# Optimization experiments

Hardware: AMD Instinct MI355X
Metric: run time of the kernel (lower is better)

The kernel has to match this reference:

```python
import jax, jax.numpy as jnp
import numpy as np

N, K, C, G, B = 65536, 16, 64, 8, 4
PE_IN = 28  # 3 + 1 + 2*4*2 + 1*4*2
EPS = 1e-5
FREQS = (1.0, 2.0, 4.0, 8.0)  # 2 ** linspace(0, 3, 4)


def _bn(x, p):
    # inference-mode BatchNorm1d over last dim; p: [4, d] = (gamma, beta, mean, var)
    return (x - p[2]) * (p[0] / jnp.sqrt(p[3] + EPS)) + p[1]


def setup_inputs() -> dict:
    key = jax.random.key(0)
    ks = iter(jax.random.split(key, 48))

    def nrm(shape, s=0.05):
        return jax.random.normal(next(ks), shape, jnp.float32) * s

    def bnp(d):
        k1, k2, k3, k4 = jax.random.split(next(ks), 4)
        return jnp.stack([
            jax.random.uniform(k1, (d,), jnp.float32, 0.5, 1.5),   # gamma
            jax.random.normal(k2, (d,), jnp.float32) * 0.1,        # beta
            jax.random.normal(k3, (d,), jnp.float32) * 0.1,        # running mean
            jax.random.uniform(k4, (d,), jnp.float32, 0.5, 1.5),   # running var
        ])

    return dict(
        feat=nrm((N, C), 1.0),
        coord=jax.random.normal(next(ks), (N, 3), jnp.float32),
        reference_index=jax.random.randint(next(ks), (N, K), 0, N),
        offset=jnp.array([N // 4, N // 2, 3 * N // 4, N], dtype=jnp.int32),
        Wq=nrm((C, C)), bq=nrm((C,)), bnq=bnp(C),
        Wk=nrm((C, C)), bk=nrm((C,)), bnk=bnp(C),
        Wv=nrm((C, C)), bv=nrm((C,)),
        pe_W1=nrm((PE_IN, C)), pe_b1=nrm((C,)), pe_bn=bnp(C),
        pe_W2=nrm((C, C)), pe_b2=nrm((C,)),
        we_W1=nrm((C, G)), we_b1=nrm((G,)), we_bn=bnp(G),
        we_W2=nrm((G, G)), we_b2=nrm((G,)),
        cg_W1=nrm((3 * C, C)), cg_b1=nrm((C,)), cg_bn=bnp(C),
        cg_W2=nrm((C, G), 0.001), cg_b2=jnp.full((G,), 3.0, jnp.float32),
    )


def reference(feat, coord, reference_index, offset, Wq, bq, bnq, Wk, bk, bnk,
              Wv, bv, pe_W1, pe_b1, pe_bn, pe_W2, pe_b2,
              we_W1, we_b1, we_bn, we_W2, we_b2,
              cg_W1, cg_b1, cg_bn, cg_W2, cg_b2):
    n = feat.shape[0]
    q = jax.nn.relu(_bn(feat @ Wq + bq, bnq))          # [N, C]
    k = jax.nn.relu(_bn(feat @ Wk + bk, bnk))          # [N, C]
    v = feat @ Wv + bv                                 # [N, C]

    idx = reference_index                              # [N, K]; -1 = pad
    idx_safe = jnp.maximum(idx, 0)
    key_feat = k[idx_safe]                             # [N, K, C] gather
    neighbor_xyz = coord[idx_safe]                     # [N, K, 3]
    value_g = v[idx_safe]                              # [N, K, C]

    delta = neighbor_xyz - coord[:, None, :]           # [N, K, 3]
    # Anisotropic Fourier relative position encoding
    x = delta.reshape(-1, 3)
    d_xy, d_z = x[:, :2], x[:, 2:3]
    dist = jnp.linalg.norm(x, axis=1, keepdims=True)
    feats = [x, dist]
    for f in FREQS:
        feats += [jnp.sin(d_xy * (f * np.pi)), jnp.cos(d_xy * (f * np.pi))]
    for f in FREQS:
        feats += [jnp.sin(d_z * (f * np.pi)), jnp.cos(d_z * (f * np.pi))]
    xe = jnp.concatenate(feats, axis=1)                # [N*K, 28]
    rpe = jax.nn.relu(_bn(xe @ pe_W1 + pe_b1, pe_bn)) @ pe_W2 + pe_b2
    rpe = rpe.reshape(n, idx.shape[1], -1)             # [N, K, C]

    relation = key_feat - q[:, None, :] + rpe          # [N, K, C]
    geom_w = jax.nn.relu(_bn(relation @ we_W1 + we_b1, we_bn)) @ we_W2 + we_b2  # [N, K, G]

    neighbor_ctx = q[idx_safe].max(axis=1)             # [N, C]
    seg = jnp.searchsorted(offset, jnp.arange(n), side='right')
    seg_max = jax.ops.segment_max(q, seg, num_segments=offset.shape[0])
    global_ctx = seg_max[seg]                          # [N, C] offset-wise global max pool

    gate_in = jnp.concatenate([q, neighbor_ctx, global_ctx], axis=-1)  # [N, 3C]
    gate = jax.nn.sigmoid(
        jax.nn.relu(_bn(gate_in @ cg_W1 + cg_b1, cg_bn)) @ cg_W2 + cg_b2)  # [N, G]

    attn = jax.nn.softmax(geom_w * gate[:, None, :], axis=1)  # softmax over K
    mask = jnp.sign(idx + 1).astype(attn.dtype)        # [N, K]
    attn = attn * mask[:, :, None]

    vg = value_g.reshape(n, idx.shape[1], G, -1)       # [N, K, G, C//G]
    out = jnp.einsum('nkgi,nkg->ngi', vg, attn)
    return out.reshape(n, -1)
```

## Files before the change

kernel.cpp:

```cpp
#include <hip/hip_runtime.h>
#include <hip/hip_bf16.h>

#define EPSF 1e-5f

typedef __attribute__((ext_vector_type(8))) short short8;
typedef __attribute__((ext_vector_type(4))) float f32x4;

__device__ __forceinline__ int seg_of(int i, int o0, int o1, int o2) {
    return (i >= o0) + (i >= o1) + (i >= o2);
}

__device__ __forceinline__ unsigned short f2bf(float f) {
    unsigned int u = __float_as_uint(f);
    unsigned int r = (u + 0x7fffu + ((u >> 16) & 1u)) >> 16;
    return (unsigned short)r;
}
__device__ __forceinline__ unsigned int pack2bf(float a, float b) {
    return (unsigned int)f2bf(a) | ((unsigned int)f2bf(b) << 16);
}
__device__ __forceinline__ float bflo(unsigned int u) { return __uint_as_float(u << 16); }
__device__ __forceinline__ float bfhi(unsigned int u) { return __uint_as_float(u & 0xffff0000u); }

__device__ __forceinline__ void stage_rows_bf16(const unsigned short* __restrict__ src,
                                                unsigned short* dst, int l) {
    int row = l >> 2, cq = (l & 3) * 16;
    const short8* s = (const short8*)(src + (size_t)row*64 + cq);
    short8* d0 = (short8*)(dst + row*72 + cq);
    d0[0] = s[0];
    d0[1] = s[1];
}

__device__ __forceinline__ void stage_rows_f32(const float* __restrict__ src,
                                               unsigned short* dst, int l) {
    int row = l >> 2, cq = (l & 3) * 16;
    const float4* s = (const float4*)(src + (size_t)row*64 + cq);
    unsigned int* d = (unsigned int*)(dst + row*72 + cq);
    #pragma unroll
    for (int i = 0; i < 4; ++i) {
        float4 f = s[i];
        d[i*2]   = pack2bf(f.x, f.y);
        d[i*2+1] = pack2bf(f.z, f.w);
    }
}

__global__ __launch_bounds__(256) void k_prep(
    const float* __restrict__ pe_W1, const float* __restrict__ pe_b1, const float* __restrict__ pe_bn,
    const float* __restrict__ pe_W2, const float* __restrict__ pe_b2,
    const float* __restrict__ we_W1, const float* __restrict__ we_b1, const float* __restrict__ we_bn,
    const float* __restrict__ cg_W1, const float* __restrict__ cg_b1, const float* __restrict__ cg_bn,
    const float* __restrict__ Wq, const float* __restrict__ bq, const float* __restrict__ bnq,
    const float* __restrict__ Wk, const float* __restrict__ bk, const float* __restrict__ bnk,
    const float* __restrict__ Wv,
    float* __restrict__ peb1f, float* __restrict__ cvecg, float* __restrict__ cgb1f,
    float* __restrict__ biasqF, float* __restrict__ biaskF, float* __restrict__ cgW1cF,
    unsigned short* __restrict__ WqF, unsigned short* __restrict__ WkF, unsigned short* __restrict__ WvF,
    unsigned short* __restrict__ weW1F, unsigned short* __restrict__ cgW1aF,
    unsigned short* __restrict__ cgW1bF,
    unsigned short* __restrict__ W1frag, unsigned short* __restrict__ Wcfrag)
{
    int t = threadIdx.x;
    __shared__ float sc1[64], csc[64], sqv[64], skv[64], wsc[8], wsh[8];
    __shared__ float sWe[64][8], sWb[8], sWc[64][8];
    if (t < 64) {
        float g = pe_bn[t], b = pe_bn[64+t], m = pe_bn[128+t], v = pe_bn[192+t];
        float s = g / sqrtf(v + EPSF);
        sc1[t] = s; peb1f[t] = pe_b1[t]*s + (b - m*s);
        g = cg_bn[t]; b = cg_bn[64+t]; m = cg_bn[128+t]; v = cg_bn[192+t];
        s = g / sqrtf(v + EPSF);
        csc[t] = s; cgb1f[t] = cg_b1[t]*s + (b - m*s);
        g = bnq[t]; b = bnq[64+t]; m = bnq[128+t]; v = bnq[192+t];
        s = g / sqrtf(v + EPSF);
        sqv[t] = s; biasqF[t] = bq[t]*s + (b - m*s);
        g = bnk[t]; b = bnk[64+t]; m = bnk[128+t]; v = bnk[192+t];
        s = g / sqrtf(v + EPSF);
        skv[t] = s; biaskF[t] = bk[t]*s + (b - m*s);
    }
    if (t < 8) {
        float g = we_bn[t], b = we_bn[8+t], m = we_bn[16+t], v = we_bn[24+t];
        float s = g / sqrtf(v + EPSF);
        wsc[t] = s; wsh[t] = b - m*s;
    }
    __syncthreads();
    for (int u = t; u < 512; u += 256) { int g = u & 7; sWe[u >> 3][g] = we_W1[u] * wsc[g]; }
    if (t < 8) sWb[t] = we_b1[t] * wsc[t] + wsh[t];
    __syncthreads();
    for (int u = t; u < 512; u += 256) {
        int h = u >> 3, g = u & 7;
        float a = 0.f;
        for (int c = 0; c < 64; ++c) a += pe_W2[h*64 + c] * sWe[c][g];
        sWc[h][g] = a;
    }
    if (t < 8) {
        float a = sWb[t];
        for (int c = 0; c < 64; ++c) a += pe_b2[c] * sWe[c][t];
        cvecg[t] = a;
    }
    __syncthreads();
    for (int u = t; u < 4096; u += 256) {
        int tile = u >> 9, l = (u >> 3) & 63, j = u & 7;
        int col = (tile >> 1)*16 + (l & 15);
        int kk  = (tile & 1)*32 + (l >> 4)*8 + j;
        WqF[u]    = f2bf(Wq[kk*64 + col] * sqv[col]);
        WkF[u]    = f2bf(Wk[kk*64 + col] * skv[col]);
        WvF[u]    = f2bf(Wv[kk*64 + col]);
        cgW1aF[u] = f2bf(cg_W1[kk*64 + col] * csc[col]);
        cgW1bF[u] = f2bf(cg_W1[(64 + kk)*64 + col] * csc[col]);
    }
    for (int u = t; u < 1024; u += 256) {
        int tile = u >> 9, l = (u >> 3) & 63, j = u & 7;
        int col = l & 15;
        int kk  = tile*32 + (l >> 4)*8 + j;
        weW1F[u] = (col < 8) ? f2bf(sWe[kk][col]) : 0;
    }
    for (int u = t; u < 4096; u += 256) {
        int k = u >> 6, c = u & 63;
        cgW1cF[u] = cg_W1[(128 + k)*64 + c] * csc[c];
    }
    {
        int ct = t >> 6, l = t & 63;
        int col = 16*ct + (l & 15), kg = l >> 4;
        #pragma unroll
        for (int j = 0; j < 8; ++j) {
            int k = kg*8 + j;
            float v = (k < 28) ? pe_W1[k*64 + col] * sc1[col] : 0.f;
            W1frag[ct*512 + l*8 + j] = f2bf(v);
        }
    }
    if (t < 128) {
        int kg = t >> 6, l = t & 63, g = l & 15;
        #pragma unroll
        for (int j = 0; j < 8; ++j) {
            int k = kg*32 + (l >> 4)*8 + j;
            float v = (g < 8) ? sWc[k][g] : 0.f;
            Wcfrag[kg*512 + l*8 + j] = f2bf(v);
        }
    }
}

__global__ __launch_bounds__(256) void k_prep2(
    const float* __restrict__ cg_W2, const float* __restrict__ we_W2,
    unsigned short* __restrict__ cgW2F, unsigned short* __restrict__ W2frag)
{
    int t = threadIdx.x;
    for (int u = t; u < 1024; u += 256) {
        int tile = u >> 9, l = (u >> 3) & 63, j = u & 7;
        int col = l & 15;
        int kk  = tile*32 + (l >> 4)*8 + j;
        cgW2F[u] = (col < 8) ? f2bf(cg_W2[kk*8 + col]) : 0;
    }
    if (t < 64) {
        int l = t, g = l & 15;
        #pragma unroll
        for (int j = 0; j < 8; ++j) {
            float v = (l < 16 && g < 8) ? we_W2[j*8 + g] : 0.f;
            W2frag[l*8 + j] = f2bf(v);
        }
    }
}

__global__ __launch_bounds__(256) void k_qkv(
    const float* __restrict__ feat, const int* __restrict__ offs,
    const unsigned short* __restrict__ WqF, const unsigned short* __restrict__ WkF,
    const unsigned short* __restrict__ WvF, const unsigned short* __restrict__ weW1F,
    const float* __restrict__ biasqF, const float* __restrict__ biaskF,
    const float* __restrict__ bv,
    unsigned short* __restrict__ v_bf, unsigned short* __restrict__ q_bf,
    float* __restrict__ kw, float* __restrict__ qw, float* __restrict__ seg_max)
{
    __shared__ unsigned short sF[4][16*72];
    __shared__ unsigned short sQ[4][16*72];
    __shared__ unsigned short sK[4][16*72];
    __shared__ float sSeg[64];

    int t = threadIdx.x, w = t >> 6, l = t & 63;
    int lc = l & 15, lg = l >> 4;
    int rblk = blockIdx.x * 64;
    int r0 = rblk + w * 16;
    int o0 = offs[0], o1 = offs[1], o2 = offs[2];
    bool fast = seg_of(rblk, o0,o1,o2) == seg_of(rblk + 63, o0,o1,o2);

    if (t < 64) sSeg[t] = 0.f;
    __syncthreads();

    stage_rows_f32(feat + (size_t)r0*64, sF[w], l);
    short8 a0 = *(const short8*)(sF[w] + lc*72 + lg*8);
    short8 a1 = *(const short8*)(sF[w] + lc*72 + 32 + lg*8);

    float bqc[4], bkc[4], bvc[4];
    #pragma unroll
    for (int ct = 0; ct < 4; ++ct) {
        bqc[ct] = biasqF[ct*16 + lc];
        bkc[ct] = biaskF[ct*16 + lc];
        bvc[ct] = bv[ct*16 + lc];
    }

    #pragma unroll
    for (int ct = 0; ct < 4; ++ct) {
        f32x4 z = {0.f,0.f,0.f,0.f};
        short8 b0 = *(const short8*)(WqF + (ct*2+0)*512 + l*8);
        short8 b1 = *(const short8*)(WqF + (ct*2+1)*512 + l*8);
        f32x4 c = __builtin_amdgcn_mfma_f32_16x16x32_bf16(a0, b0, z, 0,0,0);
        c = __builtin_amdgcn_mfma_f32_16x16x32_bf16(a1, b1, c, 0,0,0);
        float cmax = 0.f;
        #pragma unroll
        for (int reg = 0; reg < 4; ++reg) {
            float qv = fmaxf(c[reg] + bqc[ct], 0.f);
            sQ[w][(lg*4 + reg)*72 + ct*16 + lc] = f2bf(qv);
            if (fast) cmax = fmaxf(cmax, qv);
            else atomicMax((unsigned int*)&seg_max[seg_of(r0 + lg*4 + reg,o0,o1,o2)*64 + ct*16 + lc],
                           __float_as_uint(qv));
        }
        if (fast) {
            cmax = fmaxf(cmax, __shfl_xor(cmax, 16));
            cmax = fmaxf(cmax, __shfl_xor(cmax, 32));
            if (lg == 0)
                atomicMax((unsigned int*)&sSeg[ct*16 + lc], __float_as_uint(cmax));
        }
    }
    #pragma unroll
    for (int ct = 0; ct < 4; ++ct) {
        f32x4 z = {0.f,0.f,0.f,0.f};
        short8 b0 = *(const short8*)(WkF + (ct*2+0)*512 + l*8);
        short8 b1 = *(const short8*)(WkF + (ct*2+1)*512 + l*8);
        f32x4 c = __builtin_amdgcn_mfma_f32_16x16x32_bf16(a0, b0, z, 0,0,0);
        c = __builtin_amdgcn_mfma_f32_16x16x32_bf16(a1, b1, c, 0,0,0);
        #pragma unroll
        for (int reg = 0; reg < 4; ++reg)
            sK[w][(lg*4 + reg)*72 + ct*16 + lc] = f2bf(fmaxf(c[reg] + bkc[ct], 0.f));
    }
    #pragma unroll
    for (int ct = 0; ct < 4; ++ct) {
        f32x4 z = {0.f,0.f,0.f,0.f};
        short8 b0 = *(const short8*)(WvF + (ct*2+0)*512 + l*8);
        short8 b1 = *(const short8*)(WvF + (ct*2+1)*512 + l*8);
        f32x4 c = __builtin_amdgcn_mfma_f32_16x16x32_bf16(a0, b0, z, 0,0,0);
        c = __builtin_amdgcn_mfma_f32_16x16x32_bf16(a1, b1, c, 0,0,0);
        #pragma unroll
        for (int reg = 0; reg < 4; ++reg)
            sF[w][(lg*4 + reg)*72 + ct*16 + lc] = f2bf(c[reg] + bvc[ct]);
    }
    {
        short8 wb0 = *(const short8*)(weW1F + l*8);
        short8 wb1 = *(const short8*)(weW1F + 512 + l*8);
        short8 aq0 = *(const short8*)(sQ[w] + lc*72 + lg*8);
        short8 aq1 = *(const short8*)(sQ[w] + lc*72 + 32 + lg*8);
        short8 ak0 = *(const short8*)(sK[w] + lc*72 + lg*8);
        short8 ak1 = *(const short8*)(sK[w] + lc*72 + 32 + lg*8);
        f32x4 z = {0.f,0.f,0.f,0.f};
        f32x4 cq = __builtin_amdgcn_mfma_f32_16x16x32_bf16(aq0, wb0, z, 0,0,0);
        cq = __builtin_amdgcn_mfma_f32_16x16x32_bf16(aq1, wb1, cq, 0,0,0);
        f32x4 ck = __builtin_amdgcn_mfma_f32_16x16x32_bf16(ak0, wb0, z, 0,0,0);
        ck = __builtin_amdgcn_mfma_f32_16x16x32_bf16(ak1, wb1, ck, 0,0,0);
        if (lc < 8) {
            #pragma unroll
            for (int reg = 0; reg < 4; ++reg) {
                qw[(size_t)(r0 + lg*4 + reg)*8 + lc] = cq[reg];
                kw[(size_t)(r0 + lg*4 + reg)*8 + lc] = ck[reg];
            }
        }
    }
    #pragma unroll
    for (int rep = 0; rep < 2; ++rep) {
        int row = (l >> 3) + rep*8;
        int ch = (l & 7) * 8;
        short8 vq = *(const short8*)(sQ[w] + row*72 + ch);
        *(short8*)(q_bf + (size_t)(r0 + row)*64 + ch) = vq;
        short8 vv = *(const short8*)(sF[w] + row*72 + ch);
        *(short8*)(v_bf + (size_t)(r0 + row)*64 + ch) = vv;
    }
    __syncthreads();
    if (fast && t < 64)
        atomicMax((unsigned int*)&seg_max[seg_of(rblk,o0,o1,o2)*64 + t],
                  __float_as_uint(sSeg[t]));
}

__global__ __launch_bounds__(256) void k_seg(
    const float* __restrict__ seg_max, const float* __restrict__ cgW1cF,
    const float* __restrict__ cgb1f, float* __restrict__ gseg2)
{
    int t = threadIdx.x;
    int c = t & 63, s = t >> 6;
    float a = cgb1f[c];
    for (int j = 0; j < 64; ++j) a += seg_max[s*64 + j] * cgW1cF[j*64 + c];
    gseg2[s*64 + c] = a;
}

__global__ __launch_bounds__(256) void k_gate(
    const unsigned short* __restrict__ q_bf, const int* __restrict__ ridx,
    const unsigned short* __restrict__ cgW1aF, const unsigned short* __restrict__ cgW1bF,
    const unsigned short* __restrict__ cgW2F,
    const float* __restrict__ gseg2, const float* __restrict__ cg_b2,
    const int* __restrict__ offs,
    float* __restrict__ gate)
{
    __shared__ unsigned short sX[4][16*72];
    __shared__ unsigned short sN[4][16*72];
    __shared__ int sIdx[4][256];
    int t = threadIdx.x, w = t >> 6, l = t & 63;
    int lc = l & 15, lg = l >> 4;
    int r0 = blockIdx.x * 64 + w * 16;
    int o0 = offs[0], o1 = offs[1], o2 = offs[2];

    stage_rows_bf16(q_bf + (size_t)r0*64, sX[w], l);
    #pragma unroll
    for (int i = 0; i < 4; ++i)
        sIdx[w][l*4 + i] = ridx[(size_t)r0*16 + l*4 + i];

    short8 a0 = *(const short8*)(sX[w] + lc*72 + lg*8);
    short8 a1 = *(const short8*)(sX[w] + lc*72 + 32 + lg*8);

    {
        int row = l >> 2, cq = (l & 3) * 16;
        float m[16];
        #pragma unroll
        for (int i = 0; i < 16; ++i) m[i] = 0.f;
        for (int k = 0; k < 16; ++k) {
            int id = max(sIdx[w][row*16 + k], 0);
            const uint4* p = (const uint4*)(q_bf + (size_t)id*64 + cq);
            uint4 u0 = p[0], u1 = p[1];
            m[0]  = fmaxf(m[0],  bflo(u0.x)); m[1]  = fmaxf(m[1],  bfhi(u0.x));
            m[2]  = fmaxf(m[2],  bflo(u0.y)); m[3]  = fmaxf(m[3],  bfhi(u0.y));
            m[4]  = fmaxf(m[4],  bflo(u0.z)); m[5]  = fmaxf(m[5],  bfhi(u0.z));
            m[6]  = fmaxf(m[6],  bflo(u0.w)); m[7]  = fmaxf(m[7],  bfhi(u0.w));
            m[8]  = fmaxf(m[8],  bflo(u1.x)); m[9]  = fmaxf(m[9],  bfhi(u1.x));
            m[10] = fmaxf(m[10], bflo(u1.y)); m[11] = fmaxf(m[11], bfhi(u1.y));
            m[12] = fmaxf(m[12], bflo(u1.z)); m[13] = fmaxf(m[13], bfhi(u1.z));
            m[14] = fmaxf(m[14], bflo(u1.w)); m[15] = fmaxf(m[15], bfhi(u1.w));
        }
        unsigned int* d = (unsigned int*)(sN[w] + row*72 + cq);
        #pragma unroll
        for (int i = 0; i < 8; ++i) d[i] = pack2bf(m[2*i], m[2*i+1]);
    }

    f32x4 c4[4];
    #pragma unroll
    for (int ct = 0; ct < 4; ++ct) {
        #pragma unroll
        for (int reg = 0; reg < 4; ++reg)
            c4[ct][reg] = gseg2[seg_of(r0 + lg*4 + reg,o0,o1,o2)*64 + ct*16 + lc];
        short8 b0 = *(const short8*)(cgW1aF + (ct*2+0)*512 + l*8);
        short8 b1 = *(const short8*)(cgW1aF + (ct*2+1)*512 + l*8);
        c4[ct] = __builtin_amdgcn_mfma_f32_16x16x32_bf16(a0, b0, c4[ct], 0,0,0);
        c4[ct] = __builtin_amdgcn_mfma_f32_16x16x32_bf16(a1, b1, c4[ct], 0,0,0);
    }
    short8 n0v = *(const short8*)(sN[w] + lc*72 + lg*8);
    short8 n1v = *(const short8*)(sN[w] + lc*72 + 32 + lg*8);
    #pragma unroll
    for (int ct = 0; ct < 4; ++ct) {
        short8 b0 = *(const short8*)(cgW1bF + (ct*2+0)*512 + l*8);
        short8 b1 = *(const short8*)(cgW1bF + (ct*2+1)*512 + l*8);
        c4[ct] = __builtin_amdgcn_mfma_f32_16x16x32_bf16(n0v, b0, c4[ct], 0,0,0);
        c4[ct] = __builtin_amdgcn_mfma_f32_16x16x32_bf16(n1v, b1, c4[ct], 0,0,0);
        #pragma unroll
        for (int reg = 0; reg < 4; ++reg)
            sX[w][(lg*4 + reg)*72 + ct*16 + lc] = f2bf(fmaxf(c4[ct][reg], 0.f));
    }
    {
        short8 ah0 = *(const short8*)(sX[w] + lc*72 + lg*8);
        short8 ah1 = *(const short8*)(sX[w] + lc*72 + 32 + lg*8);
        short8 w0 = *(const short8*)(cgW2F + l*8);
        short8 w1 = *(const short8*)(cgW2F + 512 + l*8);
        float bg = cg_b2[lc & 7];
        f32x4 cg;
        #pragma unroll
        for (int reg = 0; reg < 4; ++reg) cg[reg] = bg;
        cg = __builtin_amdgcn_mfma_f32_16x16x32_bf16(ah0, w0, cg, 0,0,0);
        cg = __builtin_amdgcn_mfma_f32_16x16x32_bf16(ah1, w1, cg, 0,0,0);
        if (lc < 8) {
            #pragma unroll
            for (int reg = 0; reg < 4; ++reg)
                gate[(size_t)(r0 + lg*4 + reg)*8 + lc] = 1.f / (1.f + __expf(-cg[reg]));
        }
    }
}

__global__ __launch_bounds__(64, 4) void k_main(
    const float* __restrict__ coord, const int* __restrict__ ridx,
    const unsigned short* __restrict__ v_bf,
    const float* __restrict__ kw, const float* __restrict__ qw,
    const float* __restrict__ gate,
    const float* __restrict__ peb1f, const float* __restrict__ cvecg,
    const float* __restrict__ we_b2,
    const unsigned short* __restrict__ W1frag, const unsigned short* __restrict__ Wcfrag,
    const unsigned short* __restrict__ W2frag,
    float* __restrict__ out)
{
    __shared__ __align__(16) unsigned short sA1[64*40];
    __shared__ __align__(16) unsigned short sA2[16*72];
    __shared__ __align__(16) unsigned short sAh2[16*8];
    __shared__ float sAttn[4][16][9];
    __shared__ int sIds[64];

    int l = threadIdx.x;
    int pair = blockIdx.x * 64 + l;
    int nself = pair >> 4;

    int id = ridx[pair];
    sIds[l] = id;
    int ids = max(id, 0);

    {
        float cx = coord[nself*3], cy = coord[nself*3+1], cz = coord[nself*3+2];
        float dx = coord[ids*3]   - cx;
        float dy = coord[ids*3+1] - cy;
        float dz = coord[ids*3+2] - cz;
        float dist = sqrtf(dx*dx + dy*dy + dz*dz);
        unsigned int* row = (unsigned int*)sA1 + l*20;
        row[0] = pack2bf(dx, dy);
        row[1] = pack2bf(dz, dist);
        float sx, cx2, sy, cy2, sz, cz2;
        __sincosf(dx * 3.14159265358979f, &sx, &cx2);
        __sincosf(dy * 3.14159265358979f, &sy, &cy2);
        __sincosf(dz * 3.14159265358979f, &sz, &cz2);
        row[2]  = pack2bf(sx, sy);
        row[3]  = pack2bf(cx2, cy2);
        row[10] = pack2bf(sz, cz2);
        #pragma unroll
        for (int fi = 1; fi < 4; ++fi) {
            float nsx = 2.f*sx*cx2, ncx = fmaf(-2.f*sx, sx, 1.f);
            float nsy = 2.f*sy*cy2, ncy = fmaf(-2.f*sy, sy, 1.f);
            float nsz = 2.f*sz*cz2, ncz = fmaf(-2.f*sz, sz, 1.f);
            row[2 + 2*fi] = pack2bf(nsx, nsy);
            row[3 + 2*fi] = pack2bf(ncx, ncy);
            row[10 + fi]  = pack2bf(nsz, ncz);
            sx = nsx; cx2 = ncx; sy = nsy; cy2 = ncy; sz = nsz; cz2 = ncz;
        }
        row[14] = 0u; row[15] = 0u;
    }

    int lc = l & 15, lg = l >> 4;

    short8 bW1[4], bWc[2], bW2;
    #pragma unroll
    for (int ct = 0; ct < 4; ++ct) bW1[ct] = *(const short8*)(W1frag + ct*512 + l*8);
    bWc[0] = *(const short8*)(Wcfrag + l*8);
    bWc[1] = *(const short8*)(Wcfrag + 512 + l*8);
    bW2 = *(const short8*)(W2frag + l*8);

    float bias1[4];
    #pragma unroll
    for (int ct = 0; ct < 4; ++ct) bias1[ct] = peb1f[16*ct + lc];
    int g7 = lc & 7;
    float cvec_g = cvecg[g7];
    float bias3 = we_b2[g7];

    #pragma unroll
    for (int rt = 0; rt < 4; ++rt) {
        int n = blockIdx.x * 4 + rt;
        short8 a1 = *(const short8*)(sA1 + (rt*16 + lc)*40 + lg*8);
        f32x4 c1[4];
        #pragma unroll
        for (int ct = 0; ct < 4; ++ct) {
            f32x4 z = {0.f, 0.f, 0.f, 0.f};
            c1[ct] = __builtin_amdgcn_mfma_f32_16x16x32_bf16(a1, bW1[ct], z, 0, 0, 0);
        }
        #pragma unroll
        for (int ct = 0; ct < 4; ++ct) {
            #pragma unroll
            for (int reg = 0; reg < 4; ++reg) {
                float h1 = fmaxf(c1[ct][reg] + bias1[ct], 0.f);
                sA2[(lg*4 + reg)*72 + 16*ct + lc] = f2bf(h1);
            }
        }
        int ids_r[4];
        #pragma unroll
        for (int reg = 0; reg < 4; ++reg) ids_r[reg] = sIds[rt*16 + lg*4 + reg];
        float qwv = qw[(size_t)n*8 + g7];
        f32x4 c2;
        #pragma unroll
        for (int reg = 0; reg < 4; ++reg)
            c2[reg] = kw[(size_t)max(ids_r[reg],0)*8 + g7] - qwv + cvec_g;
        short8 a20 = *(const short8*)(sA2 + lc*72 + lg*8);
        short8 a21 = *(const short8*)(sA2 + lc*72 + 32 + lg*8);
        c2 = __builtin_amdgcn_mfma_f32_16x16x32_bf16(a20, bWc[0], c2, 0, 0, 0);
        c2 = __builtin_amdgcn_mfma_f32_16x16x32_bf16(a21, bWc[1], c2, 0, 0, 0);
        if (lc < 8) {
            #pragma unroll
            for (int reg = 0; reg < 4; ++reg)
                sAh2[(lg*4 + reg)*8 + lc] = f2bf(fmaxf(c2[reg], 0.f));
        }
        short8 a3 = {0,0,0,0,0,0,0,0};
        if (l < 16) a3 = *(const short8*)(sAh2 + lc*8);
        f32x4 c3;
        #pragma unroll
        for (int reg = 0; reg < 4; ++reg) c3[reg] = bias3;
        c3 = __builtin_amdgcn_mfma_f32_16x16x32_bf16(a3, bW2, c3, 0, 0, 0);
        float gv = gate[(size_t)n*8 + g7];
        float lgt[4];
        #pragma unroll
        for (int reg = 0; reg < 4; ++reg) lgt[reg] = c3[reg] * gv;
        float m = fmaxf(fmaxf(lgt[0], lgt[1]), fmaxf(lgt[2], lgt[3]));
        m = fmaxf(m, __shfl_xor(m, 16));
        m = fmaxf(m, __shfl_xor(m, 32));
        float e[4], s = 0.f;
        #pragma unroll
        for (int reg = 0; reg < 4; ++reg) { e[reg] = __expf(lgt[reg] - m); s += e[reg]; }
        s += __shfl_xor(s, 16);
        s += __shfl_xor(s, 32);
        float inv = 1.f / s;
        if (lc < 8) {
            #pragma unroll
            for (int reg = 0; reg < 4; ++reg) {
                int idv = ids_r[reg];
                float mf = (idv >= 0) ? 1.f : ((idv == -1) ? 0.f : -1.f);
                sAttn[rt][lg*4 + reg][lc] = e[reg] * inv * mf;
            }
        }
    }

    {
        int p = lg, kk = lc;
        int n2 = blockIdx.x * 4 + p;
        float4 o = make_float4(0.f, 0.f, 0.f, 0.f);
        int gh = kk >> 1;
        #pragma unroll
        for (int k2 = 0; k2 < 16; ++k2) {
            int id2 = max(sIds[p*16 + k2], 0);
            float a = sAttn[p][k2][gh];
            uint2 u = *(const uint2*)(v_bf + (size_t)id2*64 + kk*4);
            o.x += a * bflo(u.x); o.y += a * bfhi(u.x);
            o.z += a * bflo(u.y); o.w += a * bfhi(u.y);
        }
        *(float4*)(out + (size_t)n2*64 + kk*4) = o;
    }
}

extern "C" void kernel_launch(void* const* d_in, const int* in_sizes, int n_in,
                              void* d_out, int out_size, void* d_ws, size_t ws_size,
                              hipStream_t stream)
{
    const float* feat  = (const float*)d_in[0];
    const float* coord = (const float*)d_in[1];
    const int*   ridx  = (const int*)d_in[2];
    const int*   offs  = (const int*)d_in[3];
    const float* Wq = (const float*)d_in[4];  const float* bq = (const float*)d_in[5];  const float* bnq = (const float*)d_in[6];
    const float* Wk = (const float*)d_in[7];  const float* bk = (const float*)d_in[8];  const float* bnk = (const float*)d_in[9];
    const float* Wv = (const float*)d_in[10]; const float* bv = (const float*)d_in[11];
    const float* pe_W1 = (const float*)d_in[12]; const float* pe_b1 = (const float*)d_in[13]; const float* pe_bn = (const float*)d_in[14];
    const float* pe_W2 = (const float*)d_in[15]; const float* pe_b2 = (const float*)d_in[16];
    const float* we_W1 = (const float*)d_in[17]; const float* we_b1 = (const float*)d_in[18]; const float* we_bn = (const float*)d_in[19];
    const float* we_W2 = (const float*)d_in[20]; const float* we_b2 = (const float*)d_in[21];
    const float* cg_W1 = (const float*)d_in[22]; const float* cg_b1 = (const float*)d_in[23]; const float* cg_bn = (const float*)d_in[24];
    const float* cg_W2 = (const float*)d_in[25]; const float* cg_b2 = (const float*)d_in[26];
    float* out = (float*)d_out;
    int N = in_sizes[0] / 64;

    unsigned short* v_bf = (unsigned short*)d_ws;
    unsigned short* q_bf = v_bf + (size_t)N*64;
    float* kwp   = (float*)(q_bf + (size_t)N*64);
    float* qwp   = kwp + (size_t)N*8;
    float* gatep = qwp + (size_t)N*8;
    float* segm  = gatep + (size_t)N*8;
    float* gseg2 = segm + 256;
    float* peb1f = gseg2 + 256;
    float* cvecg = peb1f + 64;
    float* cgb1f = cvecg + 8;
    float* biasqF= cgb1f + 64;
    float* biaskF= biasqF + 64;
    float* pad0  = biaskF + 64;
    float* cgW1cF= pad0 + 56;
    unsigned short* WqF     = (unsigned short*)(cgW1cF + 4096);
    unsigned short* WkF     = WqF + 4096;
    unsigned short* WvF     = WkF + 4096;
    unsigned short* weW1F   = WvF + 4096;
    unsigned short* cgW1aF  = weW1F + 1024;
    unsigned short* cgW1bF  = cgW1aF + 4096;
    unsigned short* cgW2F   = cgW1bF + 4096;
    unsigned short* W1frag  = cgW2F + 1024;
    unsigned short* Wcfrag  = W1frag + 2048;
    unsigned short* W2frag  = Wcfrag + 1024;

    hipMemsetAsync(segm, 0, 256 * sizeof(float), stream);
    k_prep<<<1, 256, 0, stream>>>(pe_W1, pe_b1, pe_bn, pe_W2, pe_b2,
                                  we_W1, we_b1, we_bn,
                                  cg_W1, cg_b1, cg_bn,
                                  Wq, bq, bnq, Wk, bk, bnk, Wv,
                                  peb1f, cvecg, cgb1f, biasqF, biaskF, cgW1cF,
                                  WqF, WkF, WvF, weW1F, cgW1aF, cgW1bF,
                                  W1frag, Wcfrag);
    k_prep2<<<1, 256, 0, stream>>>(cg_W2, we_W2, cgW2F, W2frag);
    k_qkv<<<N/64, 256, 0, stream>>>(feat, offs, WqF, WkF, WvF, weW1F,
                                    biasqF, biaskF, bv,
                                    v_bf, q_bf, kwp, qwp, segm);
    k_seg<<<1, 256, 0, stream>>>(segm, cgW1cF, cgb1f, gseg2);
    k_gate<<<N/64, 256, 0, stream>>>(q_bf, ridx, cgW1aF, cgW1bF, cgW2F,
                                     gseg2, cg_b2, offs, gatep);
    k_main<<<N/4, 64, 0, stream>>>(coord, ridx, v_bf, kwp, qwp, gatep,
                                   peb1f, cvecg, we_b2,
                                   W1frag, Wcfrag, W2frag, out);
}
```

Baseline: 107.0 us.

## Fuse gate computation into main attention kernel with 256-thread blocks

Merges the separate k_gate kernel into k_main, so the context gate for each block of 16 points is computed in shared memory and read directly, with no round trip of the gate array through global memory. k_main grows from 64-thread blocks handling 4 points to 256-thread blocks handling 16 points, and the four waves split the gate's first-layer column tiles between them. This saves one launch plus the gate write and read, at the cost of extra __syncthreads barriers, more shared memory and changed occupancy (launch bounds 256,3).

```diff
diff --git a/kernel.cpp b/kernel.cpp
--- a/kernel.cpp
+++ b/kernel.cpp
@@ -285,127 +285,45 @@
     gseg2[s*64 + c] = a;
 }
 
-__global__ __launch_bounds__(256) void k_gate(
-    const unsigned short* __restrict__ q_bf, const int* __restrict__ ridx,
+__global__ __launch_bounds__(256, 3) void k_main(
+    const float* __restrict__ coord, const int* __restrict__ ridx,
+    const unsigned short* __restrict__ v_bf, const unsigned short* __restrict__ q_bf,
+    const float* __restrict__ kw, const float* __restrict__ qw,
+    const float* __restrict__ peb1f, const float* __restrict__ cvecg,
+    const float* __restrict__ we_b2, const float* __restrict__ cg_b2,
+    const float* __restrict__ gseg2, const int* __restrict__ offs,
+    const unsigned short* __restrict__ W1frag, const unsigned short* __restrict__ Wcfrag,
+    const unsigned short* __restrict__ W2frag,
     const unsigned short* __restrict__ cgW1aF, const unsigned short* __restrict__ cgW1bF,
     const unsigned short* __restrict__ cgW2F,
-    const float* __restrict__ gseg2, const float* __restrict__ cg_b2,
-    const int* __restrict__ offs,
-    float* __restrict__ gate)
+    float* __restrict__ out)
 {
-    __shared__ unsigned short sX[4][16*72];
-    __shared__ unsigned short sN[4][16*72];
-    __shared__ int sIdx[4][256];
+    __shared__ __align__(16) unsigned short sA1[256*40];
+    __shared__ __align__(16) unsigned short sA2[4][16*72];
+    __shared__ __align__(16) unsigned short sAh2[4][128];
+    __shared__ float sAttn[4][4][16][9];
+    __shared__ int sIds[256];
+    __shared__ __align__(16) unsigned short sQg[16*72];
+    __shared__ __align__(16) unsigned short sN[16*72];
+    __shared__ __align__(16) unsigned short sHg[16*72];
+    __shared__ float sGate[16][9];
+
     int t = threadIdx.x, w = t >> 6, l = t & 63;
     int lc = l & 15, lg = l >> 4;
-    int r0 = blockIdx.x * 64 + w * 16;
+    int n0 = blockIdx.x * 16;
     int o0 = offs[0], o1 = offs[1], o2 = offs[2];
 
-    stage_rows_bf16(q_bf + (size_t)r0*64, sX[w], l);
-    #pragma unroll
-    for (int i = 0; i < 4; ++i)
-        sIdx[w][l*4 + i] = ridx[(size_t)r0*16 + l*4 + i];
-
-    short8 a0 = *(const short8*)(sX[w] + lc*72 + lg*8);
-    short8 a1 = *(const short8*)(sX[w] + lc*72 + 32 + lg*8);
-
-    {
-        int row = l >> 2, cq = (l & 3) * 16;
-        float m[16];
-        #pragma unroll
-        for (int i = 0; i < 16; ++i) m[i] = 0.f;
-        for (int k = 0; k < 16; ++k) {
-            int id = max(sIdx[w][row*16 + k], 0);
-            const uint4* p = (const uint4*)(q_bf + (size_t)id*64 + cq);
-            uint4 u0 = p[0], u1 = p[1];
-            m[0]  = fmaxf(m[0],  bflo(u0.x)); m[1]  = fmaxf(m[1],  bfhi(u0.x));
-            m[2]  = fmaxf(m[2],  bflo(u0.y)); m[3]  = fmaxf(m[3],  bfhi(u0.y));
-            m[4]  = fmaxf(m[4],  bflo(u0.z)); m[5]  = fmaxf(m[5],  bfhi(u0.z));
-            m[6]  = fmaxf(m[6],  bflo(u0.w)); m[7]  = fmaxf(m[7],  bfhi(u0.w));
-            m[8]  = fmaxf(m[8],  bflo(u1.x)); m[9]  = fmaxf(m[9],  bfhi(u1.x));
-            m[10] = fmaxf(m[10], bflo(u1.y)); m[11] = fmaxf(m[11], bfhi(u1.y));
-            m[12] = fmaxf(m[12], bflo(u1.z)); m[13] = fmaxf(m[13], bfhi(u1.z));
-            m[14] = fmaxf(m[14], bflo(u1.w)); m[15] = fmaxf(m[15], bfhi(u1.w));
-        }
-        unsigned int* d = (unsigned int*)(sN[w] + row*72 + cq);
-        #pragma unroll
-        for (int i = 0; i < 8; ++i) d[i] = pack2bf(m[2*i], m[2*i+1]);
-    }
-
-    f32x4 c4[4];
-    #pragma unroll
-    for (int ct = 0; ct < 4; ++ct) {
-        #pragma unroll
-        for (int reg = 0; reg < 4; ++reg)
-            c4[ct][reg] = gseg2[seg_of(r0 + lg*4 + reg,o0,o1,o2)*64 + ct*16 + lc];
-        short8 b0 = *(const short8*)(cgW1aF + (ct*2+0)*512 + l*8);
-        short8 b1 = *(const short8*)(cgW1aF + (ct*2+1)*512 + l*8);
-        c4[ct] = __builtin_amdgcn_mfma_f32_16x16x32_bf16(a0, b0, c4[ct], 0,0,0);
-        c4[ct] = __builtin_amdgcn_mfma_f32_16x16x32_bf16(a1, b1, c4[ct], 0,0,0);
-    }
-    short8 n0v = *(const short8*)(sN[w] + lc*72 + lg*8);
-    short8 n1v = *(const short8*)(sN[w] + lc*72 + 32 + lg*8);
-    #pragma unroll
-    for (int ct = 0; ct < 4; ++ct) {
-        short8 b0 = *(const short8*)(cgW1bF + (ct*2+0)*512 + l*8);
-        short8 b1 = *(const short8*)(cgW1bF + (ct*2+1)*512 + l*8);
-        c4[ct] = __builtin_amdgcn_mfma_f32_16x16x32_bf16(n0v, b0, c4[ct], 0,0,0);
-        c4[ct] = __builtin_amdgcn_mfma_f32_16x16x32_bf16(n1v, b1, c4[ct], 0,0,0);
-        #pragma unroll
-        for (int reg = 0; reg < 4; ++reg)
-            sX[w][(lg*4 + reg)*72 + ct*16 + lc] = f2bf(fmaxf(c4[ct][reg], 0.f));
-    }
-    {
-        short8 ah0 = *(const short8*)(sX[w] + lc*72 + lg*8);
-        short8 ah1 = *(const short8*)(sX[w] + lc*72 + 32 + lg*8);
-        short8 w0 = *(const short8*)(cgW2F + l*8);
-        short8 w1 = *(const short8*)(cgW2F + 512 + l*8);
-        float bg = cg_b2[lc & 7];
-        f32x4 cg;
-        #pragma unroll
-        for (int reg = 0; reg < 4; ++reg) cg[reg] = bg;
-        cg = __builtin_amdgcn_mfma_f32_16x16x32_bf16(ah0, w0, cg, 0,0,0);
-        cg = __builtin_amdgcn_mfma_f32_16x16x32_bf16(ah1, w1, cg, 0,0,0);
-        if (lc < 8) {
-            #pragma unroll
-            for (int reg = 0; reg < 4; ++reg)
-                gate[(size_t)(r0 + lg*4 + reg)*8 + lc] = 1.f / (1.f + __expf(-cg[reg]));
-        }
-    }
-}
-
-__global__ __launch_bounds__(64, 4) void k_main(
-    const float* __restrict__ coord, const int* __restrict__ ridx,
-    const unsigned short* __restrict__ v_bf,
-    const float* __restrict__ kw, const float* __restrict__ qw,
-    const float* __restrict__ gate,
-    const float* __restrict__ peb1f, const float* __restrict__ cvecg,
-    const float* __restrict__ we_b2,
-    const unsigned short* __restrict__ W1frag, const unsigned short* __restrict__ Wcfrag,
-    const unsigned short* __restrict__ W2frag,
-    float* __restrict__ out)
-{
-    __shared__ __align__(16) unsigned short sA1[64*40];
-    __shared__ __align__(16) unsigned short sA2[16*72];
-    __shared__ __align__(16) unsigned short sAh2[16*8];
-    __shared__ float sAttn[4][16][9];
-    __shared__ int sIds[64];
-
-    int l = threadIdx.x;
-    int pair = blockIdx.x * 64 + l;
-    int nself = pair >> 4;
-
-    int id = ridx[pair];
-    sIds[l] = id;
+    int id = ridx[(size_t)n0*16 + t];
+    sIds[t] = id;
     int ids = max(id, 0);
-
+    int nself = n0 + (t >> 4);
     {
         float cx = coord[nself*3], cy = coord[nself*3+1], cz = coord[nself*3+2];
         float dx = coord[ids*3]   - cx;
         float dy = coord[ids*3+1] - cy;
         float dz = coord[ids*3+2] - cz;
         float dist = sqrtf(dx*dx + dy*dy + dz*dz);
-        unsigned int* row = (unsigned int*)sA1 + l*20;
+        unsigned int* row = (unsigned int*)sA1 + t*20;
         row[0] = pack2bf(dx, dy);
         row[1] = pack2bf(dz, dist);
         float sx, cx2, sy, cy2, sz, cz2;
@@ -427,9 +345,76 @@
         }
         row[14] = 0u; row[15] = 0u;
     }
-
-    int lc = l & 15, lg = l >> 4;
-
+    if (t < 64) stage_rows_bf16(q_bf + (size_t)n0*64, sQg, t);
+    __syncthreads();
+
+    {
+        int p = t >> 4, s = t & 15;
+        const int* ip = &sIds[p*16];
+        float m0 = 0.f, m1 = 0.f, m2 = 0.f, m3 = 0.f;
+        #pragma unroll
+        for (int kb = 0; kb < 16; kb += 4) {
+            uint2 u[4];
+            #pragma unroll
+            for (int j = 0; j < 4; ++j) {
+                int idn = max(ip[kb + j], 0);
+                u[j] = *(const uint2*)(q_bf + (size_t)idn*64 + s*4);
+            }
+            #pragma unroll
+            for (int j = 0; j < 4; ++j) {
+                m0 = fmaxf(m0, bflo(u[j].x)); m1 = fmaxf(m1, bfhi(u[j].x));
+                m2 = fmaxf(m2, bflo(u[j].y)); m3 = fmaxf(m3, bfhi(u[j].y));
+            }
+        }
+        unsigned int* d = (unsigned int*)(sN + p*72 + s*4);
+        d[0] = pack2bf(m0, m1);
+        d[1] = pack2bf(m2, m3);
+    }
+    __syncthreads();
+
+    {
+        short8 a0 = *(const short8*)(sQg + lc*72 + lg*8);
+        short8 a1 = *(const short8*)(sQg + lc*72 + 32 + lg*8);
+        short8 nv0 = *(const short8*)(sN + lc*72 + lg*8);
+        short8 nv1 = *(const short8*)(sN + lc*72 + 32 + lg*8);
+        f32x4 c4;
+        #pragma unroll
+        for (int reg = 0; reg < 4; ++reg)
+            c4[reg] = gseg2[seg_of(n0 + lg*4 + reg, o0, o1, o2)*64 + w*16 + lc];
+        short8 b0 = *(const short8*)(cgW1aF + (w*2+0)*512 + l*8);
+        short8 b1 = *(const short8*)(cgW1aF + (w*2+1)*512 + l*8);
+        c4 = __builtin_amdgcn_mfma_f32_16x16x32_bf16(a0, b0, c4, 0,0,0);
+        c4 = __builtin_amdgcn_mfma_f32_16x16x32_bf16(a1, b1, c4, 0,0,0);
+        short8 b2 = *(const short8*)(cgW1bF + (w*2+0)*512 + l*8);
+        short8 b3 = *(const short8*)(cgW1bF + (w*2+1)*512 + l*8);
+        c4 = __builtin_amdgcn_mfma_f32_16x16x32_bf16(nv0, b2, c4, 0,0,0);
+        c4 = __builtin_amdgcn_mfma_f32_16x16x32_bf16(nv1, b3, c4, 0,0,0);
+        #pragma unroll
+        for (int reg = 0; reg < 4; ++reg)
+            sHg[(lg*4 + reg)*72 + w*16 + lc] = f2bf(fmaxf(c4[reg], 0.f));
+    }
+    __syncthreads();
+
+    if (w == 0) {
+        short8 ah0 = *(const short8*)(sHg + lc*72 + lg*8);
+        short8 ah1 = *(const short8*)(sHg + lc*72 + 32 + lg*8);
+        short8 w0f = *(const short8*)(cgW2F + l*8);
+        short8 w1f = *(const short8*)(cgW2F + 512 + l*8);
+        float bg = cg_b2[lc & 7];
+        f32x4 cg;
+        #pragma unroll
+        for (int reg = 0; reg < 4; ++reg) cg[reg] = bg;
+        cg = __builtin_amdgcn_mfma_f32_16x16x32_bf16(ah0, w0f, cg, 0,0,0);
+        cg = __builtin_amdgcn_mfma_f32_16x16x32_bf16(ah1, w1f, cg, 0,0,0);
+        if (lc < 8) {
+            #pragma unroll
+            for (int reg = 0; reg < 4; ++reg)
+                sGate[lg*4 + reg][lc] = 1.f / (1.f + __expf(-cg[reg]));
+        }
+    }
+    __syncthreads();
+
+    int g7 = lc & 7;
     short8 bW1[4], bWc[2], bW2;
     #pragma unroll
     for (int ct = 0; ct < 4; ++ct) bW1[ct] = *(const short8*)(W1frag + ct*512 + l*8);
@@ -440,14 +425,13 @@
     float bias1[4];
     #pragma unroll
     for (int ct = 0; ct < 4; ++ct) bias1[ct] = peb1f[16*ct + lc];
-    int g7 = lc & 7;
     float cvec_g = cvecg[g7];
     float bias3 = we_b2[g7];
 
     #pragma unroll
     for (int rt = 0; rt < 4; ++rt) {
-        int n = blockIdx.x * 4 + rt;
-        short8 a1 = *(const short8*)(sA1 + (rt*16 + lc)*40 + lg*8);
+        int n = n0 + w*4 + rt;
+        short8 a1 = *(const short8*)(sA1 + (w*64 + rt*16 + lc)*40 + lg*8);
         f32x4 c1[4];
         #pragma unroll
         for (int ct = 0; ct < 4; ++ct) {
@@ -459,33 +443,33 @@
             #pragma unroll
             for (int reg = 0; reg < 4; ++reg) {
                 float h1 = fmaxf(c1[ct][reg] + bias1[ct], 0.f);
-                sA2[(lg*4 + reg)*72 + 16*ct + lc] = f2bf(h1);
+                sA2[w][(lg*4 + reg)*72 + 16*ct + lc] = f2bf(h1);
             }
         }
         int ids_r[4];
         #pragma unroll
-        for (int reg = 0; reg < 4; ++reg) ids_r[reg] = sIds[rt*16 + lg*4 + reg];
+        for (int reg = 0; reg < 4; ++reg) ids_r[reg] = sIds[w*64 + rt*16 + lg*4 + reg];
         float qwv = qw[(size_t)n*8 + g7];
         f32x4 c2;
         #pragma unroll
         for (int reg = 0; reg < 4; ++reg)
             c2[reg] = kw[(size_t)max(ids_r[reg],0)*8 + g7] - qwv + cvec_g;
-        short8 a20 = *(const short8*)(sA2 + lc*72 + lg*8);
-        short8 a21 = *(const short8*)(sA2 + lc*72 + 32 + lg*8);
+        short8 a20 = *(const short8*)(sA2[w] + lc*72 + lg*8);
+        short8 a21 = *(const short8*)(sA2[w] + lc*72 + 32 + lg*8);
         c2 = __builtin_amdgcn_mfma_f32_16x16x32_bf16(a20, bWc[0], c2, 0, 0, 0);
         c2 = __builtin_amdgcn_mfma_f32_16x16x32_bf16(a21, bWc[1], c2, 0, 0, 0);
         if (lc < 8) {
             #pragma unroll
             for (int reg = 0; reg < 4; ++reg)
-                sAh2[(lg*4 + reg)*8 + lc] = f2bf(fmaxf(c2[reg], 0.f));
+                sAh2[w][(lg*4 + reg)*8 + lc] = f2bf(fmaxf(c2[reg], 0.f));
         }
         short8 a3 = {0,0,0,0,0,0,0,0};
-        if (l < 16) a3 = *(const short8*)(sAh2 + lc*8);
+        if (l < 16) a3 = *(const short8*)(sAh2[w] + lc*8);
         f32x4 c3;
         #pragma unroll
         for (int reg = 0; reg < 4; ++reg) c3[reg] = bias3;
         c3 = __builtin_amdgcn_mfma_f32_16x16x32_bf16(a3, bW2, c3, 0, 0, 0);
-        float gv = gate[(size_t)n*8 + g7];
+        float gv = sGate[w*4 + rt][g7];
         float lgt[4];
         #pragma unroll
         for (int reg = 0; reg < 4; ++reg) lgt[reg] = c3[reg] * gv;
@@ -503,20 +487,20 @@
             for (int reg = 0; reg < 4; ++reg) {
                 int idv = ids_r[reg];
                 float mf = (idv >= 0) ? 1.f : ((idv == -1) ? 0.f : -1.f);
-                sAttn[rt][lg*4 + reg][lc] = e[reg] * inv * mf;
+                sAttn[w][rt][lg*4 + reg][lc] = e[reg] * inv * mf;
             }
         }
     }
 
     {
         int p = lg, kk = lc;
-        int n2 = blockIdx.x * 4 + p;
+        int n2 = n0 + w*4 + p;
         float4 o = make_float4(0.f, 0.f, 0.f, 0.f);
         int gh = kk >> 1;
         #pragma unroll
         for (int k2 = 0; k2 < 16; ++k2) {
-            int id2 = max(sIds[p*16 + k2], 0);
-            float a = sAttn[p][k2][gh];
+            int id2 = max(sIds[w*64 + p*16 + k2], 0);
+            float a = sAttn[w][p][k2][gh];
             uint2 u = *(const uint2*)(v_bf + (size_t)id2*64 + kk*4);
             o.x += a * bflo(u.x); o.y += a * bfhi(u.x);
             o.z += a * bflo(u.y); o.w += a * bfhi(u.y);
@@ -583,9 +567,8 @@
                                     biasqF, biaskF, bv,
                                     v_bf, q_bf, kwp, qwp, segm);
     k_seg<<<1, 256, 0, stream>>>(segm, cgW1cF, cgb1f, gseg2);
-    k_gate<<<N/64, 256, 0, stream>>>(q_bf, ridx, cgW1aF, cgW1bF, cgW2F,
-                                     gseg2, cg_b2, offs, gatep);
-    k_main<<<N/4, 64, 0, stream>>>(coord, ridx, v_bf, kwp, qwp, gatep,
-                                   peb1f, cvecg, we_b2,
-                                   W1frag, Wcfrag, W2frag, out);
-}
+    k_main<<<N/16, 256, 0, stream>>>(coord, ridx, v_bf, q_bf, kwp, qwp,
+                                     peb1f, cvecg, we_b2, cg_b2, gseg2, offs,
+                                     W1frag, Wcfrag, W2frag,
+                                     cgW1aF, cgW1bF, cgW2F, out);
+}
```

New measurement: 111.7 us. +4.4%, slower.
